# Optimization experiments

Hardware: AMD Instinct MI355X
Metric: run time of the kernel (lower is better)

## Reference

```python
import math
import jax, jax.numpy as jnp
import numpy as np

# ---- constants (module-level in the original source) ----
_CMAG_A = 0.75
_CMAG_B = 120.0
_CMAG_K = 17.3
_DEG2RAD = math.pi / 180.0
AMP = 100.0
_SPREAD = math.sqrt(AMP / 675.0)
VIEW_ANGLE = 90.0
MAP_SIZE = 256
SOFT_MATCH_SIGMA = 1.5
RENDER_CHUNK = 50
N_SHANK = 10            # N_CONTACTPOINTS_SHANK -> 10^3 = 1000 contacts
SPACING = 0.4           # SPACING_ALONG_XY (mm)


def setup_inputs() -> dict:
    key = jax.random.key(0)
    ks = jax.random.split(key, 12)
    B, V, N = 8, 10000, N_SHANK ** 3
    # bounded params: alpha, beta, offset, shank_length
    alpha = jax.random.uniform(ks[0], (B,), minval=-60.0, maxval=60.0)
    beta = jax.random.uniform(ks[1], (B,), minval=0.0, maxval=90.0)
    offset = jax.random.uniform(ks[2], (B,), minval=0.0, maxval=3.0)
    shank = jax.random.uniform(ks[3], (B,), minval=8.0, maxval=12.0)
    params = jnp.stack([alpha, beta, offset, shank], axis=-1).astype(jnp.float32)
    electrode_logits = jax.random.normal(ks[4], (B, N), dtype=jnp.float32)
    start_loc = jnp.array([30.0, -40.0, 10.0], dtype=jnp.float32)
    # V1 voxel positions clustered around the insertion start point
    v1_pos = start_loc + jax.random.uniform(ks[5], (V, 3), minval=-25.0, maxval=25.0)
    pol = jax.random.uniform(ks[6], (V,), minval=0.0, maxval=360.0)
    ecc = jax.random.uniform(ks[7], (V,), minval=0.2, maxval=12.0)
    sig = jax.random.uniform(ks[8], (V,), minval=0.5, maxval=3.0)
    v1_prf = jnp.stack([pol, ecc, sig], axis=-1).astype(jnp.float32)
    surf_dist_lut = jax.random.uniform(ks[9], (37, 26), minval=10.0, maxval=20.0)
    alpha_grid = jnp.linspace(-90.0, 90.0, 37, dtype=jnp.float32)
    beta_grid = jnp.linspace(-15.0, 110.0, 26, dtype=jnp.float32)
    # contact grid template [n^3, 3] = (x, y, z_frac)
    yv = jnp.arange(N_SHANK, dtype=jnp.float32) * SPACING
    xv = jnp.arange(N_SHANK, dtype=jnp.float32) * SPACING
    zf = jnp.linspace(0.0, 1.0, N_SHANK, dtype=jnp.float32)
    yy, xx, zz = jnp.meshgrid(yv, xv, zf, indexing='ij')
    grid_template = jnp.stack([xx, yy, zz], axis=-1).reshape(-1, 3)
    return {
        'params': params,
        'electrode_logits': electrode_logits,
        'v1_pos': v1_pos.astype(jnp.float32),
        'v1_prf': v1_prf,
        'start_loc': start_loc,
        'surf_dist_lut': surf_dist_lut.astype(jnp.float32),
        'alpha_grid': alpha_grid,
        'beta_grid': beta_grid,
        'grid_template': grid_template,
    }


def _rotation_matrix(alpha_deg, beta_deg):
    a = alpha_deg * _DEG2RAD
    b = beta_deg * _DEG2RAD
    ca, sa = jnp.cos(a), jnp.sin(a)
    cb, sb = jnp.cos(b), jnp.sin(b)
    ones = jnp.ones_like(a)
    zeros = jnp.zeros_like(a)
    Rx = jnp.stack([jnp.stack([ones, zeros, zeros], -1),
                    jnp.stack([zeros, ca, -sa], -1),
                    jnp.stack([zeros, sa, ca], -1)], axis=-2)
    Ry = jnp.stack([jnp.stack([cb, zeros, sb], -1),
                    jnp.stack([zeros, ones, zeros], -1),
                    jnp.stack([-sb, zeros, cb], -1)], axis=-2)
    return Rx @ Ry  # [B,3,3]


def _interp_surface_dist(alpha, beta, lut, a_grid, b_grid):
    # bilinear grid_sample with align_corners=True + border padding == clamped
    # pixel-space bilinear interpolation
    na, nb = lut.shape
    a_norm = 2.0 * (alpha - a_grid[0]) / (a_grid[-1] - a_grid[0] + 1e-08) - 1.0
    b_norm = 2.0 * (beta - b_grid[0]) / (b_grid[-1] - b_grid[0] + 1e-08) - 1.0
    ai = jnp.clip((a_norm + 1.0) * 0.5 * (na - 1), 0.0, na - 1.0)
    bi = jnp.clip((b_norm + 1.0) * 0.5 * (nb - 1), 0.0, nb - 1.0)
    a0 = jnp.clip(jnp.floor(ai), 0, na - 1).astype(jnp.int32)
    b0 = jnp.clip(jnp.floor(bi), 0, nb - 1).astype(jnp.int32)
    a1 = jnp.minimum(a0 + 1, na - 1)
    b1 = jnp.minimum(b0 + 1, nb - 1)
    fa = ai - a0.astype(ai.dtype)
    fb = bi - b0.astype(bi.dtype)
    v00 = lut[a0, b0]; v01 = lut[a0, b1]; v10 = lut[a1, b0]; v11 = lut[a1, b1]
    out = (v00 * (1 - fa) * (1 - fb) + v01 * (1 - fa) * fb
           + v10 * fa * (1 - fb) + v11 * fa * fb)
    return jnp.maximum(out, 1.0)


def _forward(params, electrode_logits, v1_pos, v1_prf, start_loc,
             surf_dist_lut, alpha_grid, beta_grid, grid_template):
    B = params.shape[0]
    N = grid_template.shape[0]
    H = W = MAP_SIZE
    alpha, beta, offset, shank = (params[:, 0], params[:, 1], params[:, 2], params[:, 3])
    elec_prob = jax.nn.sigmoid(electrode_logits)

    # ---- positioned contact grid [B,N,3] ----
    xy = jnp.broadcast_to(grid_template[None, :, :2], (B, N, 2))
    z = grid_template[None, :, 2:3] * shank[:, None, None]
    grid = jnp.concatenate([xy, z], axis=-1)
    grid = grid - grid.mean(axis=1, keepdims=True)
    R = _rotation_matrix(alpha, beta)
    rotated = jnp.einsum('bnc,bdc->bnd', grid, R)   # grid @ R^T
    ref = jnp.array([0.0, 0.0, -1.0], dtype=params.dtype)
    direction = jnp.einsum('bij,j->bi', R, ref)
    direction = direction / jnp.linalg.norm(direction, axis=-1, keepdims=True)
    surf_dist = _interp_surface_dist(alpha, beta, surf_dist_lut, alpha_grid, beta_grid)
    penetration = surf_dist - shank / 2.0 - offset
    grid_center = start_loc[None, :] + direction * penetration[:, None]
    contact_pos = rotated + grid_center[:, None, :]

    # ---- soft PRF lookup via gaussian kernel matching (avoid [B,N,V,3] diff) ----
    p2 = jnp.sum(contact_pos ** 2, axis=-1)          # [B,N]
    v2 = jnp.sum(v1_pos ** 2, axis=-1)               # [V]
    cross = jnp.einsum('bnc,vc->bnv', contact_pos, v1_pos)
    d2 = jnp.maximum(p2[:, :, None] + v2[None, None, :] - 2.0 * cross, 0.0)
    weights = jnp.exp(-d2 / (2.0 * SOFT_MATCH_SIGMA ** 2))   # [B,N,V]
    wsum = weights.sum(axis=-1)
    validity = jnp.minimum(wsum, 1.0)
    weights_norm = weights / (wsum[:, :, None] + 1e-08)
    prf = jnp.einsum('bnv,vp->bnp', weights_norm, v1_prf)    # [B,N,3]

    # ---- chunked gaussian splatting -> [B,1,H,W] ----
    angle_rad = prf[:, :, 0] * _DEG2RAD
    ecc = prf[:, :, 1]
    m = _CMAG_K * (1.0 / (ecc + _CMAG_A) - 1.0 / (ecc + _CMAG_B))
    m_inv = 1.0 / (jnp.abs(m) + 1e-08)
    phos_sigma = _SPREAD * m_inv / 2.0
    scaled_ecc = H / VIEW_ANGLE
    cx = ecc * jnp.cos(angle_rad) * scaled_ecc + H / 2.0
    cy = ecc * jnp.sin(angle_rad) * scaled_ecc + W / 2.0
    phos_size = jnp.maximum(phos_sigma * scaled_ecc, 1.0)
    w = elec_prob * validity

    gy, gx = jnp.meshgrid(jnp.arange(H, dtype=params.dtype),
                          jnp.arange(W, dtype=params.dtype), indexing='ij')
    n_chunks = N // RENDER_CHUNK
    def to_chunks(t):  # [B,N] -> [n_chunks,B,chunk]
        return t.reshape(B, n_chunks, RENDER_CHUNK).transpose(1, 0, 2)
    scan_in = (to_chunks(cx), to_chunks(cy), to_chunks(phos_size), to_chunks(w))

    def body(acc, ch):
        cx_, cy_, s_, w_ = ch  # [B,chunk]
        g = jnp.exp(-((gx[None, None] - cx_[:, :, None, None]) ** 2
                      + (gy[None, None] - cy_[:, :, None, None]) ** 2)
                    / (s_[:, :, None, None] ** 2 + 1e-08))
        return acc + jnp.einsum('bchw,bc->bhw', g, w_), None

    phos_map, _ = jax.lax.scan(body, jnp.zeros((B, H, W), dtype=params.dtype), scan_in)
    phos_map = jnp.rot90(phos_map, k=1, axes=(-2, -1))
    max_val = phos_map.reshape(B, -1).max(axis=1)[:, None, None]
    phos_map = phos_map / (max_val + 1e-08)
    return phos_map[:, None, :, :]


def reference(params, electrode_logits, v1_pos, v1_prf, start_loc,
              surf_dist_lut, alpha_grid, beta_grid, grid_template):
    return _forward(params, electrode_logits, v1_pos, v1_prf, start_loc,
                    surf_dist_lut, alpha_grid, beta_grid, grid_template)
```

## Files before the change

kernel.cpp:

```cpp
#include <hip/hip_runtime.h>
#include <math.h>

#define NB 8
#define NN 1000
#define NV 10000
#define NSEG 40
#define NSEG2 20
#define SEGCAP 256
#define NEB 1024

#define RB0 88
#define RSZ 80
#define RPX 6400
#define NEBLK 16

#define WS_CNT  0
#define WS_EPOS 512
#define WS_CPOS 33280
#define WS_CPRF 360960
#define WS_PART 524800
#define WS_MAX  1212928
#define WS_RPART 33280
#define WS_RSUM  1212936

__device__ __forceinline__ void batch_setup(const float* params, const float* start_loc,
                                            const float* lut, const float* agrid,
                                            const float* bgrid, float* sst, int t) {
    if (t < NB) {
        int b = t;
        float alpha = params[b*4+0], beta = params[b*4+1];
        float off   = params[b*4+2], shank = params[b*4+3];
        const float D2R = 0.017453292519943295f;
        float a = alpha*D2R, bb = beta*D2R;
        float ca = cosf(a), sa = sinf(a), cb = cosf(bb), sb = sinf(bb);
        float r00=cb,     r01=0.f, r02=sb;
        float r10=sa*sb,  r11=ca,  r12=-sa*cb;
        float r20=-ca*sb, r21=sa,  r22=ca*cb;
        float dx=-r02, dy=-r12, dz=-r22;
        float inv = rsqrtf(dx*dx+dy*dy+dz*dz);
        dx*=inv; dy*=inv; dz*=inv;
        float ag0=agrid[0], agN=agrid[36], bg0=bgrid[0], bgN=bgrid[25];
        float an = 2.f*(alpha-ag0)/(agN-ag0+1e-8f) - 1.f;
        float bn = 2.f*(beta -bg0)/(bgN-bg0+1e-8f) - 1.f;
        float ai = fminf(fmaxf((an+1.f)*0.5f*36.f, 0.f), 36.f);
        float bi = fminf(fmaxf((bn+1.f)*0.5f*25.f, 0.f), 25.f);
        int a0 = (int)floorf(ai); a0 = a0<0?0:(a0>36?36:a0);
        int b0 = (int)floorf(bi); b0 = b0<0?0:(b0>25?25:b0);
        int a1 = a0+1>36?36:a0+1;
        int b1 = b0+1>25?25:b0+1;
        float fa = ai - (float)a0, fb = bi - (float)b0;
        float v00=lut[a0*26+b0], v01=lut[a0*26+b1], v10=lut[a1*26+b0], v11=lut[a1*26+b1];
        float sd = v00*(1.f-fa)*(1.f-fb) + v01*(1.f-fa)*fb + v10*fa*(1.f-fb) + v11*fa*fb;
        sd = fmaxf(sd, 1.f);
        float pen = sd - shank*0.5f - off;
        float hs = shank*0.5f;
        sst[b*16+0]=r00; sst[b*16+1]=r01; sst[b*16+2]=r02;
        sst[b*16+3]=r10; sst[b*16+4]=r11; sst[b*16+5]=r12;
        sst[b*16+6]=r20; sst[b*16+7]=r21; sst[b*16+8]=r22;
        sst[b*16+9]  = start_loc[0] + dx*pen;
        sst[b*16+10] = start_loc[1] + dy*pen;
        sst[b*16+11] = start_loc[2] + dz*pen;
        sst[b*16+12] = shank;
        sst[b*16+13] = fabsf(r00)*1.8f + fabsf(r01)*1.8f + fabsf(r02)*hs;
        sst[b*16+14] = fabsf(r10)*1.8f + fabsf(r11)*1.8f + fabsf(r12)*hs;
        sst[b*16+15] = fabsf(r20)*1.8f + fabsf(r21)*1.8f + fabsf(r22)*hs;
    }
}

__global__ __launch_bounds__(256) void k_cull(const float* __restrict__ params,
                                              const float* __restrict__ start_loc,
                                              const float* __restrict__ lut,
                                              const float* __restrict__ agrid,
                                              const float* __restrict__ bgrid,
                                              const float* __restrict__ v1_pos,
                                              const float* __restrict__ v1_prf,
                                              const float* __restrict__ tmpl,
                                              float* __restrict__ ws) {
    __shared__ float sst[NB*16];
    __shared__ int   lcnt[NB];
    __shared__ float vpos[768];
    __shared__ float vprf[768];
    int g = blockIdx.x, t = threadIdx.x;
    batch_setup(params, start_loc, lut, agrid, bgrid, sst, t);
    const float C = -0.32059889797532524f;
    if (g >= NSEG) {
        if (g == NSEG && t < NB) ws[WS_MAX + t] = 0.f;
        __syncthreads();
        int v = (g - NSEG)*256 + t;
        float4* ep = (float4*)(ws + WS_EPOS);
        if (v < NB*NN) {
            int b = v/1000, n = v - b*1000;
            const float* st = sst + b*16;
            float gx = tmpl[n*3]-1.8f, gy = tmpl[n*3+1]-1.8f;
            float gz = (tmpl[n*3+2]-0.5f)*st[12];
            float px = st[0]*gx + st[1]*gy + st[2]*gz + st[9];
            float py = st[3]*gx + st[4]*gy + st[5]*gz + st[10];
            float pz = st[6]*gx + st[7]*gy + st[8]*gz + st[11];
            ep[v] = make_float4(px, py, pz, C*(px*px+py*py+pz*pz));
        } else {
            ep[v] = make_float4(0.f, 0.f, 0.f, -1e30f);
        }
        return;
    }
    if (t < NB) lcnt[t] = 0;
    #pragma unroll
    for (int k = 0; k < 3; ++k) {
        int i = k*256 + t;
        int gi = g*768 + i;
        vpos[i] = (gi < NV*3) ? v1_pos[gi] : 0.f;
        vprf[i] = (gi < NV*3) ? v1_prf[gi] : 0.f;
    }
    __syncthreads();
    int v = g*256 + t;
    bool valid = v < NV;
    float x = vpos[t*3], y = vpos[t*3+1], z = vpos[t*3+2];
    float pol = vprf[t*3], ecc = vprf[t*3+1];
    float4 payload = make_float4(-2.f*C*x, -2.f*C*y, -2.f*C*z, C*(x*x+y*y+z*z));
    int lane = t & 63;
    float4* cpos = (float4*)(ws + WS_CPOS);
    float2* cprf = (float2*)(ws + WS_CPRF);
    #pragma unroll
    for (int b = 0; b < NB; ++b) {
        const float* st = sst + b*16;
        float dxc = fmaxf(fabsf(x - st[9])  - st[13], 0.f);
        float dyc = fmaxf(fabsf(y - st[10]) - st[14], 0.f);
        float dzc = fmaxf(fabsf(z - st[11]) - st[15], 0.f);
        bool pred = valid && (dxc*dxc + dyc*dyc + dzc*dzc <= 90.f);
        unsigned long long m = __ballot(pred);
        int base = 0;
        if (lane == 0) base = atomicAdd(&lcnt[b], (int)__popcll(m));
        base = __shfl(base, 0, 64);
        if (pred) {
            int my = base + (int)__popcll(m & ((1ull << lane) - 1ull));
            int slot = b*10240 + g*SEGCAP + my;
            cpos[slot] = payload;
            cprf[slot] = make_float2(pol, ecc);
        }
    }
    __syncthreads();
    if (t < NB) ((int*)(ws + WS_CNT))[g*NB + t] = lcnt[t];
}

__global__ __launch_bounds__(256) void k_match(float* __restrict__ ws) {
    __shared__ float4 sq[2*SEGCAP];
    __shared__ float2 spe[2*SEGCAP];
    int g = blockIdx.x, t = threadIdx.x;
    int b = g / NSEG2, qp = g - b*NSEG2;
    int q0 = qp*2, q1 = q0 + 1;
    const int* cnt = (const int*)(ws + WS_CNT);
    int c0 = cnt[q0*NB + b], c1 = cnt[q1*NB + b];
    const float4* cpos = (const float4*)(ws + WS_CPOS);
    const float2* cprf = (const float2*)(ws + WS_CPRF);
    if (t < c0) {
        sq[t]  = cpos[b*10240 + q0*SEGCAP + t];
        spe[t] = cprf[b*10240 + q0*SEGCAP + t];
    }
    if (t < c1) {
        sq[c0 + t]  = cpos[b*10240 + q1*SEGCAP + t];
        spe[c0 + t] = cprf[b*10240 + q1*SEGCAP + t];
    }
    __syncthreads();
    int cq = c0 + c1;
    const float4* ep = (const float4*)(ws + WS_EPOS);
    float4 P0 = ep[b*NN + t];
    float4 P1 = (t+256 < NN) ? ep[b*NN + t+256] : make_float4(0.f,0.f,0.f,-1e30f);
    float4 P2 = (t+512 < NN) ? ep[b*NN + t+512] : make_float4(0.f,0.f,0.f,-1e30f);
    float4 P3 = (t+768 < NN) ? ep[b*NN + t+768] : make_float4(0.f,0.f,0.f,-1e30f);
    float sw0=0.f,sp0=0.f,se0=0.f, sw1=0.f,sp1=0.f,se1=0.f;
    float sw2=0.f,sp2=0.f,se2=0.f, sw3=0.f,sp3=0.f,se3=0.f;
    #pragma unroll 2
    for (int i = 0; i < cq; ++i) {
        float4 qq = sq[i];
        float2 pe = spe[i];
        float a0 = fmaf(qq.x, P0.x, fmaf(qq.y, P0.y, fmaf(qq.z, P0.z, P0.w + qq.w)));
        float w0 = __builtin_amdgcn_exp2f(a0);
        sw0 += w0; sp0 = fmaf(w0, pe.x, sp0); se0 = fmaf(w0, pe.y, se0);
        float a1 = fmaf(qq.x, P1.x, fmaf(qq.y, P1.y, fmaf(qq.z, P1.z, P1.w + qq.w)));
        float w1 = __builtin_amdgcn_exp2f(a1);
        sw1 += w1; sp1 = fmaf(w1, pe.x, sp1); se1 = fmaf(w1, pe.y, se1);
        float a2 = fmaf(qq.x, P2.x, fmaf(qq.y, P2.y, fmaf(qq.z, P2.z, P2.w + qq.w)));
        float w2 = __builtin_amdgcn_exp2f(a2);
        sw2 += w2; sp2 = fmaf(w2, pe.x, sp2); se2 = fmaf(w2, pe.y, se2);
        float a3 = fmaf(qq.x, P3.x, fmaf(qq.y, P3.y, fmaf(qq.z, P3.z, P3.w + qq.w)));
        float w3 = __builtin_amdgcn_exp2f(a3);
        sw3 += w3; sp3 = fmaf(w3, pe.x, sp3); se3 = fmaf(w3, pe.y, se3);
    }
    float4* part = (float4*)(ws + WS_PART);
    int baseq = (b*NSEG2 + qp)*NEB;
    part[baseq + t]       = make_float4(sw0, sp0, se0, 0.f);
    part[baseq + t + 256] = make_float4(sw1, sp1, se1, 0.f);
    part[baseq + t + 512] = make_float4(sw2, sp2, se2, 0.f);
    part[baseq + t + 768] = make_float4(sw3, sp3, se3, 0.f);
}

__global__ __launch_bounds__(256) void k_render(const float* __restrict__ logits,
                                                float* __restrict__ ws) {
    __shared__ float reg[RPX];
    __shared__ float4 red[4][64];
    __shared__ float4 spar[64];
    int g = blockIdx.x, t = threadIdx.x, lane = t & 63, w = t >> 6;
    int b = g >> 4, eb = g & 15, E0 = eb*64;
    for (int i = t; i < RPX; i += 256) reg[i] = 0.f;
    const float4* part = (const float4*)(ws + WS_PART);
    int el = E0 + lane;
    {
        float sw = 0.f, sp = 0.f, se = 0.f;
        #pragma unroll
        for (int i = 0; i < 5; ++i) {
            float4 p = part[(b*NSEG2 + (w + i*4))*NEB + el];
            sw += p.x; sp += p.y; se += p.z;
        }
        red[w][lane] = make_float4(sw, sp, se, 0.f);
    }
    __syncthreads();
    if (w == 0) {
        float4 a = red[0][lane], b4 = red[1][lane], c4 = red[2][lane], d4 = red[3][lane];
        float sw = (a.x+b4.x) + (c4.x+d4.x);
        float sp = (a.y+b4.y) + (c4.y+d4.y);
        float se = (a.z+b4.z) + (c4.z+d4.z);
        float denom = sw + 1e-8f;
        float pol = sp/denom, eccv = se/denom;
        float validity = fminf(sw, 1.f);
        int n = E0 + lane;
        float lg = (n < NN) ? logits[b*NN + n] : 0.f;
        float prob = 1.f/(1.f + __expf(-lg));
        float wgt = (n < NN) ? prob * validity : 0.f;
        float ang = pol * 0.017453292519943295f;
        float m1 = 17.3f*(1.f/(eccv+0.75f) - 1.f/(eccv+120.f));
        float minv = 1.f/(fabsf(m1)+1e-8f);
        float sig  = 0.3849001794597506f * minv * 0.5f;
        const float scl = 256.f/90.f;
        float s = fmaxf(sig*scl, 1.f);
        float invden = 1.f/(s*s + 1e-8f);
        spar[lane] = make_float4(eccv*__cosf(ang)*scl + 128.f,
                                 eccv*__sinf(ang)*scl + 128.f, invden, wgt);
    }
    __syncthreads();
    int ix = lane & 7, iy = lane >> 3;
    #pragma unroll
    for (int k = 0; k < 16; ++k) {
        float4 P = spar[k*4 + w];
        if (P.w <= 0.f) continue;
        int fx = (int)floorf(P.x), fy = (int)floorf(P.y);
        int X = fx - 3 + ix, Y = fy - 3 + iy;
        int xl = X - RB0, yl = Y - RB0;
        float dx = (float)X - P.x, dy = (float)Y - P.y;
        float d2 = dx*dx + dy*dy;
        if ((unsigned)xl < RSZ && (unsigned)yl < RSZ && d2 <= 12.25f) {
            atomicAdd(&reg[xl*RSZ + yl], P.w * __expf(-d2 * P.z));
        }
    }
    __syncthreads();
    float4* dst = (float4*)(ws + WS_RPART) + g*(RPX/4);
    const float4* src = (const float4*)reg;
    #pragma unroll
    for (int i = 0; i < 7; ++i) {
        int idx = i*256 + t;
        if (idx < RPX/4) dst[idx] = src[idx];
    }
}

__global__ __launch_bounds__(256) void k_sum(float* __restrict__ ws) {
    __shared__ float mred[4];
    int g = blockIdx.x, t = threadIdx.x, lane = t & 63, w = t >> 6;
    int b = g / 25, p25 = g - b*25;
    int px = p25*256 + t;
    const float* rp = ws + WS_RPART + (b*NEBLK)*RPX + px;
    float s = 0.f;
    #pragma unroll
    for (int p = 0; p < NEBLK; ++p) s += rp[p*RPX];
    ws[WS_RSUM + b*RPX + px] = s;
    float mx = s;
    #pragma unroll
    for (int s2 = 32; s2 >= 1; s2 >>= 1) mx = fmaxf(mx, __shfl_xor(mx, s2, 64));
    if (lane == 0) mred[w] = mx;
    __syncthreads();
    if (t == 0) {
        mx = fmaxf(fmaxf(mred[0], mred[1]), fmaxf(mred[2], mred[3]));
        atomicMax((unsigned int*)(ws + WS_MAX + b), __float_as_uint(mx));
    }
}

__global__ __launch_bounds__(256) void k_out(const float* __restrict__ ws,
                                             float* __restrict__ out) {
    int o = blockIdx.x*256 + threadIdx.x;
    int b = o >> 14, rem = o & 16383;
    int r = rem >> 6, c4 = (rem & 63) << 2;
    float inv = 1.f/(ws[WS_MAX + b] + 1e-8f);
    float4 v = make_float4(0.f, 0.f, 0.f, 0.f);
    int xl = 167 - r;
    if ((unsigned)xl < RSZ) {
        const float* rs = ws + WS_RSUM + b*RPX + xl*RSZ;
        float* vv = &v.x;
        #pragma unroll
        for (int j = 0; j < 4; ++j) {
            int yl = c4 + j - RB0;
            if ((unsigned)yl < RSZ) vv[j] = rs[yl]*inv;
        }
    }
    ((float4*)out)[o] = v;
}

extern "C" void kernel_launch(void* const* d_in, const int* in_sizes, int n_in,
                              void* d_out, int out_size, void* d_ws, size_t ws_size,
                              hipStream_t stream) {
    const float* params    = (const float*)d_in[0];
    const float* logits    = (const float*)d_in[1];
    const float* v1_pos    = (const float*)d_in[2];
    const float* v1_prf    = (const float*)d_in[3];
    const float* start_loc = (const float*)d_in[4];
    const float* lut       = (const float*)d_in[5];
    const float* agrid     = (const float*)d_in[6];
    const float* bgrid     = (const float*)d_in[7];
    const float* tmpl      = (const float*)d_in[8];
    float* ws  = (float*)d_ws;
    float* out = (float*)d_out;

    k_cull  <<<72,  256, 0, stream>>>(params, start_loc, lut, agrid, bgrid,
                                      v1_pos, v1_prf, tmpl, ws);
    k_match <<<160, 256, 0, stream>>>(ws);
    k_render<<<128, 256, 0, stream>>>(logits, ws);
    k_sum   <<<200, 256, 0, stream>>>(ws);
    k_out   <<<512, 256, 0, stream>>>(ws, out);
}
```

Baseline: 103.6 us.

## Fuse culling into match kernel and replace partial-sum pass with global atomics

The culling stage moves into the match kernel. Each block computes its own batch setup, filters its 512 voxels directly into shared memory, and computes electrode positions in registers, which removes the cull launch and the workspace round-trip. The separate reduction kernel is also removed. Render blocks now atomically add their nonzero region pixels into a zeroed global sum and track the per-batch max from the atomic return values. Atomic contention and redundant per-block setup replace two kernel launches and the partial-buffer traffic. The max taken from intermediate atomic values is still correct, because the final sum is the largest value reached and all contributions are positive.

```diff
diff --git a/kernel.cpp b/kernel.cpp
--- a/kernel.cpp
+++ b/kernel.cpp
@@ -4,184 +4,134 @@
 #define NB 8
 #define NN 1000
 #define NV 10000
-#define NSEG 40
 #define NSEG2 20
-#define SEGCAP 256
 #define NEB 1024
 
 #define RB0 88
 #define RSZ 80
 #define RPX 6400
-#define NEBLK 16
-
-#define WS_CNT  0
-#define WS_EPOS 512
-#define WS_CPOS 33280
-#define WS_CPRF 360960
-#define WS_PART 524800
-#define WS_MAX  1212928
-#define WS_RPART 33280
-#define WS_RSUM  1212936
-
-__device__ __forceinline__ void batch_setup(const float* params, const float* start_loc,
-                                            const float* lut, const float* agrid,
-                                            const float* bgrid, float* sst, int t) {
-    if (t < NB) {
-        int b = t;
-        float alpha = params[b*4+0], beta = params[b*4+1];
-        float off   = params[b*4+2], shank = params[b*4+3];
-        const float D2R = 0.017453292519943295f;
-        float a = alpha*D2R, bb = beta*D2R;
-        float ca = cosf(a), sa = sinf(a), cb = cosf(bb), sb = sinf(bb);
-        float r00=cb,     r01=0.f, r02=sb;
-        float r10=sa*sb,  r11=ca,  r12=-sa*cb;
-        float r20=-ca*sb, r21=sa,  r22=ca*cb;
-        float dx=-r02, dy=-r12, dz=-r22;
-        float inv = rsqrtf(dx*dx+dy*dy+dz*dz);
-        dx*=inv; dy*=inv; dz*=inv;
-        float ag0=agrid[0], agN=agrid[36], bg0=bgrid[0], bgN=bgrid[25];
-        float an = 2.f*(alpha-ag0)/(agN-ag0+1e-8f) - 1.f;
-        float bn = 2.f*(beta -bg0)/(bgN-bg0+1e-8f) - 1.f;
-        float ai = fminf(fmaxf((an+1.f)*0.5f*36.f, 0.f), 36.f);
-        float bi = fminf(fmaxf((bn+1.f)*0.5f*25.f, 0.f), 25.f);
-        int a0 = (int)floorf(ai); a0 = a0<0?0:(a0>36?36:a0);
-        int b0 = (int)floorf(bi); b0 = b0<0?0:(b0>25?25:b0);
-        int a1 = a0+1>36?36:a0+1;
-        int b1 = b0+1>25?25:b0+1;
-        float fa = ai - (float)a0, fb = bi - (float)b0;
-        float v00=lut[a0*26+b0], v01=lut[a0*26+b1], v10=lut[a1*26+b0], v11=lut[a1*26+b1];
-        float sd = v00*(1.f-fa)*(1.f-fb) + v01*(1.f-fa)*fb + v10*fa*(1.f-fb) + v11*fa*fb;
-        sd = fmaxf(sd, 1.f);
-        float pen = sd - shank*0.5f - off;
-        float hs = shank*0.5f;
-        sst[b*16+0]=r00; sst[b*16+1]=r01; sst[b*16+2]=r02;
-        sst[b*16+3]=r10; sst[b*16+4]=r11; sst[b*16+5]=r12;
-        sst[b*16+6]=r20; sst[b*16+7]=r21; sst[b*16+8]=r22;
-        sst[b*16+9]  = start_loc[0] + dx*pen;
-        sst[b*16+10] = start_loc[1] + dy*pen;
-        sst[b*16+11] = start_loc[2] + dz*pen;
-        sst[b*16+12] = shank;
-        sst[b*16+13] = fabsf(r00)*1.8f + fabsf(r01)*1.8f + fabsf(r02)*hs;
-        sst[b*16+14] = fabsf(r10)*1.8f + fabsf(r11)*1.8f + fabsf(r12)*hs;
-        sst[b*16+15] = fabsf(r20)*1.8f + fabsf(r21)*1.8f + fabsf(r22)*hs;
-    }
-}
-
-__global__ __launch_bounds__(256) void k_cull(const float* __restrict__ params,
-                                              const float* __restrict__ start_loc,
-                                              const float* __restrict__ lut,
-                                              const float* __restrict__ agrid,
-                                              const float* __restrict__ bgrid,
-                                              const float* __restrict__ v1_pos,
-                                              const float* __restrict__ v1_prf,
-                                              const float* __restrict__ tmpl,
-                                              float* __restrict__ ws) {
-    __shared__ float sst[NB*16];
-    __shared__ int   lcnt[NB];
-    __shared__ float vpos[768];
-    __shared__ float vprf[768];
-    int g = blockIdx.x, t = threadIdx.x;
-    batch_setup(params, start_loc, lut, agrid, bgrid, sst, t);
+
+#define WS_PART 0
+#define WS_RSUM 655360
+#define WS_MAX  706560
+
+__device__ __forceinline__ void batch_setup_one(const float* params, const float* start_loc,
+                                                const float* lut, const float* agrid,
+                                                const float* bgrid, float* sst, int b) {
+    float alpha = params[b*4+0], beta = params[b*4+1];
+    float off   = params[b*4+2], shank = params[b*4+3];
+    const float D2R = 0.017453292519943295f;
+    float a = alpha*D2R, bb = beta*D2R;
+    float ca = cosf(a), sa = sinf(a), cb = cosf(bb), sb = sinf(bb);
+    float r00=cb,     r01=0.f, r02=sb;
+    float r10=sa*sb,  r11=ca,  r12=-sa*cb;
+    float r20=-ca*sb, r21=sa,  r22=ca*cb;
+    float dx=-r02, dy=-r12, dz=-r22;
+    float inv = rsqrtf(dx*dx+dy*dy+dz*dz);
+    dx*=inv; dy*=inv; dz*=inv;
+    float ag0=agrid[0], agN=agrid[36], bg0=bgrid[0], bgN=bgrid[25];
+    float an = 2.f*(alpha-ag0)/(agN-ag0+1e-8f) - 1.f;
+    float bn = 2.f*(beta -bg0)/(bgN-bg0+1e-8f) - 1.f;
+    float ai = fminf(fmaxf((an+1.f)*0.5f*36.f, 0.f), 36.f);
+    float bi = fminf(fmaxf((bn+1.f)*0.5f*25.f, 0.f), 25.f);
+    int a0 = (int)floorf(ai); a0 = a0<0?0:(a0>36?36:a0);
+    int b0 = (int)floorf(bi); b0 = b0<0?0:(b0>25?25:b0);
+    int a1 = a0+1>36?36:a0+1;
+    int b1 = b0+1>25?25:b0+1;
+    float fa = ai - (float)a0, fb = bi - (float)b0;
+    float v00=lut[a0*26+b0], v01=lut[a0*26+b1], v10=lut[a1*26+b0], v11=lut[a1*26+b1];
+    float sd = v00*(1.f-fa)*(1.f-fb) + v01*(1.f-fa)*fb + v10*fa*(1.f-fb) + v11*fa*fb;
+    sd = fmaxf(sd, 1.f);
+    float pen = sd - shank*0.5f - off;
+    float hs = shank*0.5f;
+    sst[0]=r00; sst[1]=r01; sst[2]=r02;
+    sst[3]=r10; sst[4]=r11; sst[5]=r12;
+    sst[6]=r20; sst[7]=r21; sst[8]=r22;
+    sst[9]  = start_loc[0] + dx*pen;
+    sst[10] = start_loc[1] + dy*pen;
+    sst[11] = start_loc[2] + dz*pen;
+    sst[12] = shank;
+    sst[13] = fabsf(r00)*1.8f + fabsf(r01)*1.8f + fabsf(r02)*hs;
+    sst[14] = fabsf(r10)*1.8f + fabsf(r11)*1.8f + fabsf(r12)*hs;
+    sst[15] = fabsf(r20)*1.8f + fabsf(r21)*1.8f + fabsf(r22)*hs;
+}
+
+__global__ __launch_bounds__(256) void k_match(const float* __restrict__ params,
+                                               const float* __restrict__ start_loc,
+                                               const float* __restrict__ lut,
+                                               const float* __restrict__ agrid,
+                                               const float* __restrict__ bgrid,
+                                               const float* __restrict__ v1_pos,
+                                               const float* __restrict__ v1_prf,
+                                               const float* __restrict__ tmpl,
+                                               float* __restrict__ ws) {
+    __shared__ float4 sq[512];
+    __shared__ float2 spe[512];
+    __shared__ float  sst[16];
+    __shared__ int    scnt;
+    int g = blockIdx.x, t = threadIdx.x, lane = t & 63;
+    int b = g / NSEG2, qp = g - b*NSEG2;
+    for (int i = g*256 + t; i < NB*RPX; i += 160*256) ws[WS_RSUM + i] = 0.f;
+    if (g == 0 && t < NB) ws[WS_MAX + t] = 0.f;
+    if (t == 0) { batch_setup_one(params, start_loc, lut, agrid, bgrid, sst, b); scnt = 0; }
+    __syncthreads();
     const float C = -0.32059889797532524f;
-    if (g >= NSEG) {
-        if (g == NSEG && t < NB) ws[WS_MAX + t] = 0.f;
-        __syncthreads();
-        int v = (g - NSEG)*256 + t;
-        float4* ep = (float4*)(ws + WS_EPOS);
-        if (v < NB*NN) {
-            int b = v/1000, n = v - b*1000;
-            const float* st = sst + b*16;
-            float gx = tmpl[n*3]-1.8f, gy = tmpl[n*3+1]-1.8f;
-            float gz = (tmpl[n*3+2]-0.5f)*st[12];
-            float px = st[0]*gx + st[1]*gy + st[2]*gz + st[9];
-            float py = st[3]*gx + st[4]*gy + st[5]*gz + st[10];
-            float pz = st[6]*gx + st[7]*gy + st[8]*gz + st[11];
-            ep[v] = make_float4(px, py, pz, C*(px*px+py*py+pz*pz));
-        } else {
-            ep[v] = make_float4(0.f, 0.f, 0.f, -1e30f);
-        }
-        return;
-    }
-    if (t < NB) lcnt[t] = 0;
-    #pragma unroll
-    for (int k = 0; k < 3; ++k) {
-        int i = k*256 + t;
-        int gi = g*768 + i;
-        vpos[i] = (gi < NV*3) ? v1_pos[gi] : 0.f;
-        vprf[i] = (gi < NV*3) ? v1_prf[gi] : 0.f;
-    }
-    __syncthreads();
-    int v = g*256 + t;
-    bool valid = v < NV;
-    float x = vpos[t*3], y = vpos[t*3+1], z = vpos[t*3+2];
-    float pol = vprf[t*3], ecc = vprf[t*3+1];
-    float4 payload = make_float4(-2.f*C*x, -2.f*C*y, -2.f*C*z, C*(x*x+y*y+z*z));
-    int lane = t & 63;
-    float4* cpos = (float4*)(ws + WS_CPOS);
-    float2* cprf = (float2*)(ws + WS_CPRF);
-    #pragma unroll
-    for (int b = 0; b < NB; ++b) {
-        const float* st = sst + b*16;
-        float dxc = fmaxf(fabsf(x - st[9])  - st[13], 0.f);
-        float dyc = fmaxf(fabsf(y - st[10]) - st[14], 0.f);
-        float dzc = fmaxf(fabsf(z - st[11]) - st[15], 0.f);
+    #pragma unroll
+    for (int h = 0; h < 2; ++h) {
+        int v = qp*512 + h*256 + t;
+        bool valid = v < NV;
+        float x=0.f, y=0.f, z=0.f, pol=0.f, ecc=0.f;
+        if (valid) {
+            x = v1_pos[v*3]; y = v1_pos[v*3+1]; z = v1_pos[v*3+2];
+            pol = v1_prf[v*3]; ecc = v1_prf[v*3+1];
+        }
+        float dxc = fmaxf(fabsf(x - sst[9])  - sst[13], 0.f);
+        float dyc = fmaxf(fabsf(y - sst[10]) - sst[14], 0.f);
+        float dzc = fmaxf(fabsf(z - sst[11]) - sst[15], 0.f);
         bool pred = valid && (dxc*dxc + dyc*dyc + dzc*dzc <= 90.f);
         unsigned long long m = __ballot(pred);
         int base = 0;
-        if (lane == 0) base = atomicAdd(&lcnt[b], (int)__popcll(m));
+        if (lane == 0) base = atomicAdd(&scnt, (int)__popcll(m));
         base = __shfl(base, 0, 64);
         if (pred) {
-            int my = base + (int)__popcll(m & ((1ull << lane) - 1ull));
-            int slot = b*10240 + g*SEGCAP + my;
-            cpos[slot] = payload;
-            cprf[slot] = make_float2(pol, ecc);
-        }
-    }
-    __syncthreads();
-    if (t < NB) ((int*)(ws + WS_CNT))[g*NB + t] = lcnt[t];
-}
-
-__global__ __launch_bounds__(256) void k_match(float* __restrict__ ws) {
-    __shared__ float4 sq[2*SEGCAP];
-    __shared__ float2 spe[2*SEGCAP];
-    int g = blockIdx.x, t = threadIdx.x;
-    int b = g / NSEG2, qp = g - b*NSEG2;
-    int q0 = qp*2, q1 = q0 + 1;
-    const int* cnt = (const int*)(ws + WS_CNT);
-    int c0 = cnt[q0*NB + b], c1 = cnt[q1*NB + b];
-    const float4* cpos = (const float4*)(ws + WS_CPOS);
-    const float2* cprf = (const float2*)(ws + WS_CPRF);
-    if (t < c0) {
-        sq[t]  = cpos[b*10240 + q0*SEGCAP + t];
-        spe[t] = cprf[b*10240 + q0*SEGCAP + t];
-    }
-    if (t < c1) {
-        sq[c0 + t]  = cpos[b*10240 + q1*SEGCAP + t];
-        spe[c0 + t] = cprf[b*10240 + q1*SEGCAP + t];
-    }
-    __syncthreads();
-    int cq = c0 + c1;
-    const float4* ep = (const float4*)(ws + WS_EPOS);
-    float4 P0 = ep[b*NN + t];
-    float4 P1 = (t+256 < NN) ? ep[b*NN + t+256] : make_float4(0.f,0.f,0.f,-1e30f);
-    float4 P2 = (t+512 < NN) ? ep[b*NN + t+512] : make_float4(0.f,0.f,0.f,-1e30f);
-    float4 P3 = (t+768 < NN) ? ep[b*NN + t+768] : make_float4(0.f,0.f,0.f,-1e30f);
+            int idx = base + (int)__popcll(m & ((1ull << lane) - 1ull));
+            sq[idx]  = make_float4(-2.f*C*x, -2.f*C*y, -2.f*C*z, C*(x*x+y*y+z*z));
+            spe[idx] = make_float2(pol, ecc);
+        }
+    }
+    float4 P[4];
+    #pragma unroll
+    for (int j = 0; j < 4; ++j) {
+        int n = t + j*256;
+        if (n < NN) {
+            float gx = tmpl[n*3]-1.8f, gy = tmpl[n*3+1]-1.8f;
+            float gz = (tmpl[n*3+2]-0.5f)*sst[12];
+            float px = sst[0]*gx + sst[1]*gy + sst[2]*gz + sst[9];
+            float py = sst[3]*gx + sst[4]*gy + sst[5]*gz + sst[10];
+            float pz = sst[6]*gx + sst[7]*gy + sst[8]*gz + sst[11];
+            P[j] = make_float4(px, py, pz, C*(px*px+py*py+pz*pz));
+        } else {
+            P[j] = make_float4(0.f, 0.f, 0.f, -1e30f);
+        }
+    }
+    __syncthreads();
+    int cq = scnt;
     float sw0=0.f,sp0=0.f,se0=0.f, sw1=0.f,sp1=0.f,se1=0.f;
     float sw2=0.f,sp2=0.f,se2=0.f, sw3=0.f,sp3=0.f,se3=0.f;
     #pragma unroll 2
     for (int i = 0; i < cq; ++i) {
         float4 qq = sq[i];
         float2 pe = spe[i];
-        float a0 = fmaf(qq.x, P0.x, fmaf(qq.y, P0.y, fmaf(qq.z, P0.z, P0.w + qq.w)));
+        float a0 = fmaf(qq.x, P[0].x, fmaf(qq.y, P[0].y, fmaf(qq.z, P[0].z, P[0].w + qq.w)));
         float w0 = __builtin_amdgcn_exp2f(a0);
         sw0 += w0; sp0 = fmaf(w0, pe.x, sp0); se0 = fmaf(w0, pe.y, se0);
-        float a1 = fmaf(qq.x, P1.x, fmaf(qq.y, P1.y, fmaf(qq.z, P1.z, P1.w + qq.w)));
+        float a1 = fmaf(qq.x, P[1].x, fmaf(qq.y, P[1].y, fmaf(qq.z, P[1].z, P[1].w + qq.w)));
         float w1 = __builtin_amdgcn_exp2f(a1);
         sw1 += w1; sp1 = fmaf(w1, pe.x, sp1); se1 = fmaf(w1, pe.y, se1);
-        float a2 = fmaf(qq.x, P2.x, fmaf(qq.y, P2.y, fmaf(qq.z, P2.z, P2.w + qq.w)));
+        float a2 = fmaf(qq.x, P[2].x, fmaf(qq.y, P[2].y, fmaf(qq.z, P[2].z, P[2].w + qq.w)));
         float w2 = __builtin_amdgcn_exp2f(a2);
         sw2 += w2; sp2 = fmaf(w2, pe.x, sp2); se2 = fmaf(w2, pe.y, se2);
-        float a3 = fmaf(qq.x, P3.x, fmaf(qq.y, P3.y, fmaf(qq.z, P3.z, P3.w + qq.w)));
+        float a3 = fmaf(qq.x, P[3].x, fmaf(qq.y, P[3].y, fmaf(qq.z, P[3].z, P[3].w + qq.w)));
         float w3 = __builtin_amdgcn_exp2f(a3);
         sw3 += w3; sp3 = fmaf(w3, pe.x, sp3); se3 = fmaf(w3, pe.y, se3);
     }
@@ -198,6 +148,7 @@
     __shared__ float reg[RPX];
     __shared__ float4 red[4][64];
     __shared__ float4 spar[64];
+    __shared__ float mred[4];
     int g = blockIdx.x, t = threadIdx.x, lane = t & 63, w = t >> 6;
     int b = g >> 4, eb = g & 15, E0 = eb*64;
     for (int i = t; i < RPX; i += 256) reg[i] = 0.f;
@@ -239,38 +190,27 @@
     int ix = lane & 7, iy = lane >> 3;
     #pragma unroll
     for (int k = 0; k < 16; ++k) {
-        float4 P = spar[k*4 + w];
-        if (P.w <= 0.f) continue;
-        int fx = (int)floorf(P.x), fy = (int)floorf(P.y);
+        float4 Pp = spar[k*4 + w];
+        if (Pp.w <= 0.f) continue;
+        int fx = (int)floorf(Pp.x), fy = (int)floorf(Pp.y);
         int X = fx - 3 + ix, Y = fy - 3 + iy;
         int xl = X - RB0, yl = Y - RB0;
-        float dx = (float)X - P.x, dy = (float)Y - P.y;
+        float dx = (float)X - Pp.x, dy = (float)Y - Pp.y;
         float d2 = dx*dx + dy*dy;
         if ((unsigned)xl < RSZ && (unsigned)yl < RSZ && d2 <= 12.25f) {
-            atomicAdd(&reg[xl*RSZ + yl], P.w * __expf(-d2 * P.z));
-        }
-    }
-    __syncthreads();
-    float4* dst = (float4*)(ws + WS_RPART) + g*(RPX/4);
-    const float4* src = (const float4*)reg;
-    #pragma unroll
-    for (int i = 0; i < 7; ++i) {
-        int idx = i*256 + t;
-        if (idx < RPX/4) dst[idx] = src[idx];
-    }
-}
-
-__global__ __launch_bounds__(256) void k_sum(float* __restrict__ ws) {
-    __shared__ float mred[4];
-    int g = blockIdx.x, t = threadIdx.x, lane = t & 63, w = t >> 6;
-    int b = g / 25, p25 = g - b*25;
-    int px = p25*256 + t;
-    const float* rp = ws + WS_RPART + (b*NEBLK)*RPX + px;
-    float s = 0.f;
-    #pragma unroll
-    for (int p = 0; p < NEBLK; ++p) s += rp[p*RPX];
-    ws[WS_RSUM + b*RPX + px] = s;
-    float mx = s;
+            atomicAdd(&reg[xl*RSZ + yl], Pp.w * __expf(-d2 * Pp.z));
+        }
+    }
+    __syncthreads();
+    float* rsum = ws + WS_RSUM + b*RPX;
+    float mx = 0.f;
+    for (int i = t; i < RPX; i += 256) {
+        float v = reg[i];
+        if (v > 0.f) {
+            float old = atomicAdd(&rsum[i], v);
+            mx = fmaxf(mx, old + v);
+        }
+    }
     #pragma unroll
     for (int s2 = 32; s2 >= 1; s2 >>= 1) mx = fmaxf(mx, __shfl_xor(mx, s2, 64));
     if (lane == 0) mred[w] = mx;
@@ -316,10 +256,8 @@
     float* ws  = (float*)d_ws;
     float* out = (float*)d_out;
 
-    k_cull  <<<72,  256, 0, stream>>>(params, start_loc, lut, agrid, bgrid,
+    k_match <<<160, 256, 0, stream>>>(params, start_loc, lut, agrid, bgrid,
                                       v1_pos, v1_prf, tmpl, ws);
-    k_match <<<160, 256, 0, stream>>>(ws);
     k_render<<<128, 256, 0, stream>>>(logits, ws);
-    k_sum   <<<200, 256, 0, stream>>>(ws);
     k_out   <<<512, 256, 0, stream>>>(ws, out);
 }
```

Result: faster. 98.88 us (median of 2 runs) (-4.6%).
